# Optimization experiments

Hardware: AMD Instinct MI355X
Metric: run time of the kernel (lower is better)

The kernel has to match this reference:

```python
import jax, jax.numpy as jnp
import numpy as np

HEADS = 20
HEAD_DIM = 64
IP_WEIGHT = 1.0

def _sdpa(q, k, v):
    # q: [b,h,sq,d], k/v: [b,h,skv,d]
    scale = 1.0 / np.sqrt(q.shape[-1])
    logits = jnp.einsum('bhqd,bhkd->bhqk', q, k) * scale
    probs = jax.nn.softmax(logits, axis=-1)
    return jnp.einsum('bhqk,bhkd->bhqd', probs, v)

def _split_heads(t, b, h, d):
    return t.reshape(b, -1, h, d).transpose(0, 2, 1, 3)

def setup_inputs() -> dict:
    key = jax.random.key(0)
    ks = jax.random.split(key, 10)
    B, S, D, C, T = 4, 4096, 1280, 2048, 16
    def w(k, fan_in, shape):
        return jax.random.normal(k, shape, dtype=jnp.float32) / np.sqrt(fan_in)
    return {
        'x': jax.random.normal(ks[0], (B, S, D), dtype=jnp.float32),
        'context': jax.random.normal(ks[1], (B, 77, C), dtype=jnp.float32),
        'image_emb': jax.random.normal(ks[2], (B, T, C), dtype=jnp.float32),
        'Wq': w(ks[3], D, (D, D)),
        'Wk': w(ks[4], C, (C, D)),
        'Wv': w(ks[5], C, (C, D)),
        'Wk_ip': w(ks[6], C, (C, D)),
        'Wv_ip': w(ks[7], C, (C, D)),
        'Wo': w(ks[8], D, (D, D)),
        'bo': jnp.zeros((D,), dtype=jnp.float32),
    }

def reference(x, context, image_emb, Wq, Wk, Wv, Wk_ip, Wv_ip, Wo, bo):
    b, s, inner = x.shape
    h, d = HEADS, HEAD_DIM
    q = _split_heads(x @ Wq, b, h, d)            # [b,h,s,d]
    k = _split_heads(context @ Wk, b, h, d)      # [b,h,77,d]
    v = _split_heads(context @ Wv, b, h, d)
    out = _sdpa(q, k, v)                         # main cross-attn
    ip_k = _split_heads(image_emb @ Wk_ip, b, h, d)  # [b,h,16,d]
    ip_v = _split_heads(image_emb @ Wv_ip, b, h, d)
    ip_out = _sdpa(q, ip_k, ip_v)                # image-conditioned attn, same q
    out = out + IP_WEIGHT * ip_out
    out = out.transpose(0, 2, 1, 3).reshape(b, s, h * d)
    return out @ Wo + bo
```

## Files before the change

### kernel.cpp

```cpp
#include <hip/hip_runtime.h>
#include <cstdint>

typedef __bf16 bf16;
typedef __bf16 bf16x8 __attribute__((ext_vector_type(8)));
typedef float f32x4 __attribute__((ext_vector_type(4)));

#define MFMA16(a, b, c) __builtin_amdgcn_mfma_f32_16x16x32_bf16((a), (b), (c), 0, 0, 0)
#define GLDS16(g, l)                                                         \
  __builtin_amdgcn_global_load_lds(                                          \
      (__attribute__((address_space(1))) void*)(g),                          \
      (__attribute__((address_space(3))) void*)(l), 16, 0, 0)

__global__ void prep_all(const float* __restrict__ Wq, const float* __restrict__ Wo,
                         const float* __restrict__ Wk, const float* __restrict__ Wv,
                         const float* __restrict__ Wkip, const float* __restrict__ Wvip,
                         bf16* __restrict__ WqT, bf16* __restrict__ WoT,
                         bf16* __restrict__ WkT, bf16* __restrict__ WvT,
                         bf16* __restrict__ WkipT, bf16* __restrict__ WvipT,
                         const float* __restrict__ x, bf16* __restrict__ xb,
                         const float* __restrict__ ctx, bf16* __restrict__ ctxb,
                         const float* __restrict__ img, bf16* __restrict__ imgb) {
  const int z = blockIdx.z;
  const int tx = threadIdx.x, ty = threadIdx.y;
  if (z < 6) {
    const float* src = (z == 0) ? Wq : (z == 1) ? Wo : (z == 2) ? Wk
                      : (z == 3) ? Wv : (z == 4) ? Wkip : Wvip;
    bf16* dst = (z == 0) ? WqT : (z == 1) ? WoT : (z == 2) ? WkT
               : (z == 3) ? WvT : (z == 4) ? WkipT : WvipT;
    const int K = (z < 2) ? 1280 : 2048;
    const int N = 1280;
    __shared__ float t[32][33];
    const int bx = blockIdx.x * 32, by = blockIdx.y * 32;
    if (by >= K) return;
#pragma unroll
    for (int i = 0; i < 32; i += 8)
      t[ty + i][tx] = src[(long)(by + ty + i) * N + bx + tx];
    __syncthreads();
#pragma unroll
    for (int i = 0; i < 32; i += 8)
      dst[(long)(bx + ty + i) * K + by + tx] = (bf16)t[tx][ty + i];
    return;
  }
  const int tid = ty * 32 + tx;
  const int bid = blockIdx.y * 40 + blockIdx.x;
  const float* s;
  bf16* d;
  long base;
  if (z < 10) {
    base = (((long)(z - 6) * 2560 + bid) * 256 + tid) * 8;
    s = x; d = xb;
  } else if (bid < 308) {
    base = ((long)bid * 256 + tid) * 8;
    s = ctx; d = ctxb;
  } else if (bid < 372) {
    base = ((long)(bid - 308) * 256 + tid) * 8;
    s = img; d = imgb;
  } else {
    return;
  }
  float4 a = *(const float4*)(s + base);
  float4 b = *(const float4*)(s + base + 4);
  bf16x8 o;
  o[0] = (bf16)a.x; o[1] = (bf16)a.y; o[2] = (bf16)a.z; o[3] = (bf16)a.w;
  o[4] = (bf16)b.x; o[5] = (bf16)b.y; o[6] = (bf16)b.z; o[7] = (bf16)b.w;
  *(bf16x8*)(d + base) = o;
}

template <bool OUT_BF16, bool HAS_BIAS>
__device__ __forceinline__ void gemm_bt_core(const bf16* A, const bf16* Bt,
                                             void* Cp, const float* bias,
                                             int K, int N, int tm, int tn) {
  __shared__ bf16 Al[3][128 * 32];
  __shared__ bf16 Bl[3][128 * 32];
  const int tid = threadIdx.x;
  const int wave = tid >> 6, lane = tid & 63;
  const int g = lane >> 4, l16 = lane & 15;

  const int sr = lane >> 2;
  const int sc = ((lane & 3) ^ ((lane >> 3) & 3)) * 8;
  const bf16* ga0 = A + (long)(tm + wave * 16 + sr) * K + sc;
  const bf16* ga1 = ga0 + (long)64 * K;
  const bf16* gb0 = Bt + (long)(tn + wave * 16 + sr) * K + sc;
  const bf16* gb1 = gb0 + (long)64 * K;

  f32x4 acc[4][4] = {};
  const int wr = (wave >> 1) * 64, wc = (wave & 1) * 64;
  const int rsw = (g ^ ((l16 >> 1) & 3)) * 8;
  const int paOfs = (wr + l16) * 32 + rsw;
  const int pbOfs = (wc + l16) * 32 + rsw;

  const int NT = K >> 5;

#define STAGE_TILE(t_, b_)                              \
  {                                                     \
    const int kt_ = (t_) << 5;                          \
    GLDS16(ga0 + kt_, &Al[b_][wave * 512]);             \
    GLDS16(ga1 + kt_, &Al[b_][(wave + 4) * 512]);       \
    GLDS16(gb0 + kt_, &Bl[b_][wave * 512]);             \
    GLDS16(gb1 + kt_, &Bl[b_][(wave + 4) * 512]);       \
  }

#define READS(sl_, af_, bf_)                                      \
  {                                                               \
    const bf16* pa_ = &Al[sl_][paOfs];                            \
    const bf16* pb_ = &Bl[sl_][pbOfs];                            \
    _Pragma("unroll") for (int i_ = 0; i_ < 4; i_++)              \
        af_[i_] = *(const bf16x8*)(pa_ + i_ * 16 * 32);           \
    _Pragma("unroll") for (int j_ = 0; j_ < 4; j_++)              \
        bf_[j_] = *(const bf16x8*)(pb_ + j_ * 16 * 32);           \
  }

  STAGE_TILE(0, 0);
  STAGE_TILE(1, 1);
  asm volatile("s_waitcnt vmcnt(4)" ::: "memory");
  asm volatile("s_barrier" ::: "memory");
  bf16x8 afA[4], bfA[4], afB[4], bfB[4];
  READS(0, afA, bfA);
  int slc = 0;

#define GEMM_ITER(t_, afC, bfC, afN, bfN)                         \
  {                                                               \
    asm volatile("s_waitcnt lgkmcnt(0)" ::: "memory");            \
    __builtin_amdgcn_sched_barrier(0);                            \
    if ((t_) + 2 < NT) {                                          \
      const int snx_ = (slc + 2 >= 3) ? slc - 1 : slc + 2;        \
      STAGE_TILE((t_) + 2, snx_);                                 \
      asm volatile("s_waitcnt vmcnt(4)" ::: "memory");            \
    } else if ((t_) + 1 < NT) {                                   \
      asm volatile("s_waitcnt vmcnt(0)" ::: "memory");            \
    }                                                             \
    asm volatile("s_barrier" ::: "memory");                       \
    const int srd_ = (slc + 1 >= 3) ? 0 : slc + 1;                \
    if ((t_) + 1 < NT) READS(srd_, afN, bfN);                     \
    __builtin_amdgcn_sched_barrier(0);                            \
    __builtin_amdgcn_s_setprio(1);                                \
    _Pragma("unroll") for (int i_ = 0; i_ < 4; i_++)              \
        _Pragma("unroll") for (int j_ = 0; j_ < 4; j_++)          \
            acc[i_][j_] = MFMA16(afC[i_], bfC[j_], acc[i_][j_]);  \
    __builtin_amdgcn_s_setprio(0);                                \
    slc = srd_;                                                   \
  }

  for (int t = 0; t < NT; t += 2) {
    GEMM_ITER(t, afA, bfA, afB, bfB);
    GEMM_ITER(t + 1, afB, bfB, afA, bfA);
  }
#undef GEMM_ITER
#undef READS
#undef STAGE_TILE

#pragma unroll
  for (int i = 0; i < 4; i++) {
#pragma unroll
    for (int j = 0; j < 4; j++) {
      const int col = tn + wc + j * 16 + l16;
      float bv = 0.f;
      if (HAS_BIAS) bv = bias[col];
#pragma unroll
      for (int r = 0; r < 4; r++) {
        const long row = (long)tm + wr + i * 16 + g * 4 + r;
        float v = acc[i][j][r] + bv;
        if (OUT_BF16)
          ((bf16*)Cp)[row * N + col] = (bf16)v;
        else
          ((float*)Cp)[row * N + col] = v;
      }
    }
  }
}

__global__ __launch_bounds__(256) void gemm_qproj_small(
    const bf16* __restrict__ xb, const bf16* __restrict__ WqT,
    bf16* __restrict__ qb, const bf16* __restrict__ ctxb,
    const bf16* __restrict__ imgb, const bf16* __restrict__ WkT,
    const bf16* __restrict__ WvT, const bf16* __restrict__ WkipT,
    const bf16* __restrict__ WvipT, bf16* __restrict__ kb,
    bf16* __restrict__ vb, bf16* __restrict__ ipkb, bf16* __restrict__ ipvb) {
  const int i = blockIdx.x;
  const bf16 *A, *Bt;
  bf16* C;
  int K, tm, tn;
  if (i >= 80) {
    const int q = i - 80;
    const int local = q >> 3;
    A = xb; Bt = WqT; C = qb; K = 1280;
    tm = ((q & 7) * 16 + local / 10) * 128;
    tn = (local % 10) * 128;
  } else {
    int z, bx, by;
    if (i < 60) {
      z = i / 30;
      const int r = i % 30;
      bx = r % 3;
      by = r / 3;
    } else {
      z = 2 + (i - 60) / 10;
      bx = 0;
      by = (i - 60) % 10;
    }
    A = (z < 2) ? ctxb : imgb;
    Bt = (z == 0) ? WkT : (z == 1) ? WvT : (z == 2) ? WkipT : WvipT;
    C = (z == 0) ? kb : (z == 1) ? vb : (z == 2) ? ipkb : ipvb;
    K = 2048;
    tm = bx * 128;
    tn = by * 128;
  }
  gemm_bt_core<true, false>(A, Bt, C, nullptr, K, 1280, tm, tn);
}

__global__ __launch_bounds__(256) void gemm_f32out_bias(
    const bf16* __restrict__ A, const bf16* __restrict__ Bt,
    float* __restrict__ C, const float* __restrict__ bias, int K, int N) {
  const int i = blockIdx.x;
  const int local = i >> 3;
  const int tm = ((i & 7) * 16 + local / 10) * 128;
  const int tn = (local % 10) * 128;
  gemm_bt_core<false, true>(A, Bt, C, bias, K, N, tm, tn);
}

__global__ __launch_bounds__(256) void attention_kernel(
    const bf16* __restrict__ q, const bf16* __restrict__ k,
    const bf16* __restrict__ v, const bf16* __restrict__ ipk,
    const bf16* __restrict__ ipv, bf16* __restrict__ out) {
  __shared__ bf16 Kl[96 * 64];
  __shared__ bf16 Vt[64 * 104];
  __shared__ bf16 Pl[4][16 * 104];

  const int b = blockIdx.z, h = blockIdx.y, qblk = blockIdx.x;
  const int tid = threadIdx.x;

  {
    uint32_t* vz = (uint32_t*)Vt;
    for (int i = tid; i < 64 * 104 / 2; i += 256) vz[i] = 0;
  }
  __syncthreads();

  for (int c = tid; c < 77 * 8; c += 256) {
    const int row = c >> 3, d0 = (c & 7) * 8;
    const long src = (long)(b * 77 + row) * 1280 + h * 64 + d0;
    bf16x8 kk = *(const bf16x8*)&k[src];
    *(bf16x8*)&Kl[row * 64 + (d0 ^ ((row & 7) << 3))] = kk;
    bf16x8 vv = *(const bf16x8*)&v[src];
#pragma unroll
    for (int i2 = 0; i2 < 8; i2++) Vt[(d0 + i2) * 104 + row] = vv[i2];
  }
  if (tid < 16 * 8) {
    const int r = tid >> 3, d0 = (tid & 7) * 8;
    const int row = 80 + r;
    const long src = (long)(b * 16 + r) * 1280 + h * 64 + d0;
    bf16x8 kk = *(const bf16x8*)&ipk[src];
    *(bf16x8*)&Kl[row * 64 + (d0 ^ ((row & 7) << 3))] = kk;
    bf16x8 vv = *(const bf16x8*)&ipv[src];
#pragma unroll
    for (int i2 = 0; i2 < 8; i2++) Vt[(d0 + i2) * 104 + row] = vv[i2];
  }
  __syncthreads();

  const int wave = tid >> 6, lane = tid & 63;
  const int g = lane >> 4, l16 = lane & 15;
  const float sc = 0.125f * 1.44269504f;

  for (int it = 0; it < 2; it++) {
    const long qrow = (long)b * 4096 + qblk * 128 + wave * 32 + it * 16;
    bf16x8 qf[2];
#pragma unroll
    for (int ks = 0; ks < 2; ks++)
      qf[ks] = *(const bf16x8*)&q[(qrow + l16) * 1280 + h * 64 + ks * 32 + g * 8];

    f32x4 lt[6];
#pragma unroll
    for (int t = 0; t < 6; t++) {
      f32x4 a = {0.f, 0.f, 0.f, 0.f};
#pragma unroll
      for (int ks = 0; ks < 2; ks++) {
        const int row = t * 16 + l16;
        const int d = (ks * 32 + g * 8) ^ ((row & 7) << 3);
        bf16x8 kb8 = *(const bf16x8*)&Kl[row * 64 + d];
        a = MFMA16(qf[ks], kb8, a);
      }
      lt[t] = a;
    }

    float p[6][4];
#pragma unroll
    for (int r = 0; r < 4; r++) {
      float lv[5], m = -3e38f;
#pragma unroll
      for (int t = 0; t < 5; t++) {
        const int kv = t * 16 + l16;
        lv[t] = (kv < 77) ? lt[t][r] * sc : -3e38f;
        m = fmaxf(m, lv[t]);
      }
      for (int msk = 1; msk < 16; msk <<= 1) m = fmaxf(m, __shfl_xor(m, msk, 16));
      float s = 0.f;
#pragma unroll
      for (int t = 0; t < 5; t++) {
        const float pp = exp2f(lv[t] - m);
        p[t][r] = pp;
        s += pp;
      }
      for (int msk = 1; msk < 16; msk <<= 1) s += __shfl_xor(s, msk, 16);
      const float inv = 1.f / s;
#pragma unroll
      for (int t = 0; t < 5; t++) p[t][r] *= inv;
      const float l5 = lt[5][r] * sc;
      float m2 = l5;
      for (int msk = 1; msk < 16; msk <<= 1) m2 = fmaxf(m2, __shfl_xor(m2, msk, 16));
      const float p5 = exp2f(l5 - m2);
      float s2 = p5;
      for (int msk = 1; msk < 16; msk <<= 1) s2 += __shfl_xor(s2, msk, 16);
      p[5][r] = p5 / s2;
    }

#pragma unroll
    for (int t = 0; t < 6; t++)
#pragma unroll
      for (int r = 0; r < 4; r++)
        Pl[wave][(g * 4 + r) * 104 + t * 16 + l16] = (bf16)p[t][r];
    __syncthreads();

    bf16x8 paf[3];
#pragma unroll
    for (int ks = 0; ks < 3; ks++)
      paf[ks] = *(const bf16x8*)&Pl[wave][l16 * 104 + ks * 32 + g * 8];
#pragma unroll
    for (int n = 0; n < 4; n++) {
      f32x4 o = {0.f, 0.f, 0.f, 0.f};
#pragma unroll
      for (int ks = 0; ks < 3; ks++) {
        bf16x8 vbf = *(const bf16x8*)&Vt[(n * 16 + l16) * 104 + ks * 32 + g * 8];
        o = MFMA16(paf[ks], vbf, o);
      }
#pragma unroll
      for (int r = 0; r < 4; r++)
        out[(qrow + g * 4 + r) * 1280 + h * 64 + n * 16 + l16] = (bf16)o[r];
    }
    __syncthreads();
  }
}

extern "C" void kernel_launch(void* const* d_in, const int* in_sizes, int n_in,
                              void* d_out, int out_size, void* d_ws,
                              size_t ws_size, hipStream_t stream) {
  const float* x = (const float*)d_in[0];
  const float* ctx = (const float*)d_in[1];
  const float* img = (const float*)d_in[2];
  const float* Wq = (const float*)d_in[3];
  const float* Wk = (const float*)d_in[4];
  const float* Wv = (const float*)d_in[5];
  const float* Wkip = (const float*)d_in[6];
  const float* Wvip = (const float*)d_in[7];
  const float* Wo = (const float*)d_in[8];
  const float* bo = (const float*)d_in[9];
  float* out = (float*)d_out;

  bf16* ws = (bf16*)d_ws;
  size_t o = 0;
  auto alloc = [&](size_t n) { bf16* p = ws + o; o += n; return p; };
  bf16* xattn = alloc(16384L * 1280);
  bf16* qb    = alloc(16384L * 1280);
  bf16* WqT   = alloc(1280L * 1280);
  bf16* WoT   = alloc(1280L * 1280);
  bf16* WkT   = alloc(1280L * 2048);
  bf16* WvT   = alloc(1280L * 2048);
  bf16* WkipT = alloc(1280L * 2048);
  bf16* WvipT = alloc(1280L * 2048);
  bf16* ctxb  = alloc(384L * 2048);
  bf16* imgb  = alloc(128L * 2048);
  bf16* kb    = alloc(384L * 1280);
  bf16* vb    = alloc(384L * 1280);
  bf16* ipkb  = alloc(128L * 1280);
  bf16* ipvb  = alloc(128L * 1280);

  prep_all<<<dim3(40, 64, 11), dim3(32, 8), 0, stream>>>(
      Wq, Wo, Wk, Wv, Wkip, Wvip, WqT, WoT, WkT, WvT, WkipT, WvipT, x, xattn,
      ctx, ctxb, img, imgb);

  gemm_qproj_small<<<1360, 256, 0, stream>>>(xattn, WqT, qb, ctxb, imgb, WkT,
                                             WvT, WkipT, WvipT, kb, vb, ipkb,
                                             ipvb);

  attention_kernel<<<dim3(32, 20, 4), 256, 0, stream>>>(qb, kb, vb, ipkb, ipvb,
                                                        xattn);

  gemm_f32out_bias<<<1280, 256, 0, stream>>>(xattn, WoT, out, bo, 1280, 1280);
}
```

Before: 232.2 us.

## Switch projection GEMMs to 256x256 tiles with 512-thread blocks and BK=64

Replaces the 128x128, 256-thread, triple-buffered GEMM core with a 256x256 tile per 512-thread block. It uses K-steps of 64 and double-buffered LDS, and interleaves the next tile's global-to-LDS loads between four MFMA sub-phases. The larger tile raises arithmetic intensity and operand reuse per LDS load. It also adds row guards so the small K/V projections can use the bigger tile. In exchange, grids shrink to 350 and 320 blocks, leaving a partial second wave on 256 CUs. The 128 KB of LDS per block limits occupancy, and the padded small-M tiles read past the logical end of ctx/img rows.

New measurement: 264.3 us. +13.8%, slower.

```diff
diff --git a/kernel.cpp b/kernel.cpp
--- a/kernel.cpp
+++ b/kernel.cpp
@@ -67,109 +67,160 @@
 }
 
 template <bool OUT_BF16, bool HAS_BIAS>
-__device__ __forceinline__ void gemm_bt_core(const bf16* A, const bf16* Bt,
+__device__ __forceinline__ void gemm256_core(const bf16* A, const bf16* Bt,
                                              void* Cp, const float* bias,
-                                             int K, int N, int tm, int tn) {
-  __shared__ bf16 Al[3][128 * 32];
-  __shared__ bf16 Bl[3][128 * 32];
+                                             int K, int N, int tm, int tn,
+                                             int Mlim) {
+  __shared__ bf16 Al[2][16384];
+  __shared__ bf16 Bl[2][16384];
   const int tid = threadIdx.x;
   const int wave = tid >> 6, lane = tid & 63;
   const int g = lane >> 4, l16 = lane & 15;
-
-  const int sr = lane >> 2;
-  const int sc = ((lane & 3) ^ ((lane >> 3) & 3)) * 8;
-  const bf16* ga0 = A + (long)(tm + wave * 16 + sr) * K + sc;
-  const bf16* ga1 = ga0 + (long)64 * K;
-  const bf16* gb0 = Bt + (long)(tn + wave * 16 + sr) * K + sc;
-  const bf16* gb1 = gb0 + (long)64 * K;
-
-  f32x4 acc[4][4] = {};
-  const int wr = (wave >> 1) * 64, wc = (wave & 1) * 64;
-  const int rsw = (g ^ ((l16 >> 1) & 3)) * 8;
-  const int paOfs = (wr + l16) * 32 + rsw;
-  const int pbOfs = (wc + l16) * 32 + rsw;
-
-  const int NT = K >> 5;
-
-#define STAGE_TILE(t_, b_)                              \
-  {                                                     \
-    const int kt_ = (t_) << 5;                          \
-    GLDS16(ga0 + kt_, &Al[b_][wave * 512]);             \
-    GLDS16(ga1 + kt_, &Al[b_][(wave + 4) * 512]);       \
-    GLDS16(gb0 + kt_, &Bl[b_][wave * 512]);             \
-    GLDS16(gb1 + kt_, &Bl[b_][(wave + 4) * 512]);       \
-  }
-
-#define READS(sl_, af_, bf_)                                      \
+  const int wr = wave >> 2, wc = wave & 3;
+
+  const int srow = wave * 16 + (lane >> 3);
+  const int scol = ((lane & 7) ^ ((lane >> 3) & 7)) * 8;
+  const bf16* gA = A + (long)(tm + srow) * K + scol;
+  const bf16* gB = Bt + (long)(tn + srow) * K + scol;
+  const int ldst = wave * 1024;
+
+#define STAGE_HALF(Lb_, gp_, b_, hh_, t_)                         \
   {                                                               \
-    const bf16* pa_ = &Al[sl_][paOfs];                            \
-    const bf16* pb_ = &Bl[sl_][pbOfs];                            \
-    _Pragma("unroll") for (int i_ = 0; i_ < 4; i_++)              \
-        af_[i_] = *(const bf16x8*)(pa_ + i_ * 16 * 32);           \
-    _Pragma("unroll") for (int j_ = 0; j_ < 4; j_++)              \
-        bf_[j_] = *(const bf16x8*)(pb_ + j_ * 16 * 32);           \
-  }
-
-  STAGE_TILE(0, 0);
-  STAGE_TILE(1, 1);
-  asm volatile("s_waitcnt vmcnt(4)" ::: "memory");
+    const bf16* s_ = (gp_) + (long)(hh_) * 128 * K + (t_) * 64;   \
+    GLDS16(s_, &Lb_[b_][(hh_)*8192 + ldst]);                      \
+    GLDS16(s_ + 8 * K, &Lb_[b_][(hh_)*8192 + ldst + 512]);        \
+  }
+
+  const int cs0 = (g ^ (l16 & 7)) * 8;
+  const int cs1 = ((4 + g) ^ (l16 & 7)) * 8;
+  const int aB0 = (wr * 64 + l16) * 64;
+  const int aB1 = aB0 + 8192;
+  const int bB = (wc * 64 + l16) * 64;
+
+  f32x4 acc[8][4] = {};
+  bf16x8 aF[4][2], bF[4][2];
+
+  const int NT = K >> 6;
+
+  STAGE_HALF(Al, gA, 0, 0, 0);
+  STAGE_HALF(Al, gA, 0, 1, 0);
+  STAGE_HALF(Bl, gB, 0, 0, 0);
+  STAGE_HALF(Bl, gB, 0, 1, 0);
+  STAGE_HALF(Al, gA, 1, 0, 1);
+  STAGE_HALF(Bl, gB, 1, 0, 1);
+  STAGE_HALF(Bl, gB, 1, 1, 1);
+  asm volatile("s_waitcnt vmcnt(6)" ::: "memory");
   asm volatile("s_barrier" ::: "memory");
-  bf16x8 afA[4], bfA[4], afB[4], bfB[4];
-  READS(0, afA, bfA);
-  int slc = 0;
-
-#define GEMM_ITER(t_, afC, bfC, afN, bfN)                         \
-  {                                                               \
-    asm volatile("s_waitcnt lgkmcnt(0)" ::: "memory");            \
-    __builtin_amdgcn_sched_barrier(0);                            \
-    if ((t_) + 2 < NT) {                                          \
-      const int snx_ = (slc + 2 >= 3) ? slc - 1 : slc + 2;        \
-      STAGE_TILE((t_) + 2, snx_);                                 \
-      asm volatile("s_waitcnt vmcnt(4)" ::: "memory");            \
-    } else if ((t_) + 1 < NT) {                                   \
-      asm volatile("s_waitcnt vmcnt(0)" ::: "memory");            \
-    }                                                             \
-    asm volatile("s_barrier" ::: "memory");                       \
-    const int srd_ = (slc + 1 >= 3) ? 0 : slc + 1;                \
-    if ((t_) + 1 < NT) READS(srd_, afN, bfN);                     \
-    __builtin_amdgcn_sched_barrier(0);                            \
-    __builtin_amdgcn_s_setprio(1);                                \
-    _Pragma("unroll") for (int i_ = 0; i_ < 4; i_++)              \
-        _Pragma("unroll") for (int j_ = 0; j_ < 4; j_++)          \
-            acc[i_][j_] = MFMA16(afC[i_], bfC[j_], acc[i_][j_]);  \
-    __builtin_amdgcn_s_setprio(0);                                \
-    slc = srd_;                                                   \
-  }
-
-  for (int t = 0; t < NT; t += 2) {
-    GEMM_ITER(t, afA, bfA, afB, bfB);
-    GEMM_ITER(t + 1, afB, bfB, afA, bfA);
-  }
-#undef GEMM_ITER
-#undef READS
-#undef STAGE_TILE
-
-#pragma unroll
-  for (int i = 0; i < 4; i++) {
-#pragma unroll
-    for (int j = 0; j < 4; j++) {
-      const int col = tn + wc + j * 16 + l16;
+
+  for (int t = 0; t < NT; ++t) {
+    const int b = t & 1;
+#pragma unroll
+    for (int mi = 0; mi < 4; ++mi) {
+      aF[mi][0] = *(const bf16x8*)&Al[b][aB0 + mi * 1024 + cs0];
+      aF[mi][1] = *(const bf16x8*)&Al[b][aB0 + mi * 1024 + cs1];
+    }
+#pragma unroll
+    for (int nj = 0; nj < 2; ++nj) {
+      bF[nj][0] = *(const bf16x8*)&Bl[b][bB + nj * 1024 + cs0];
+      bF[nj][1] = *(const bf16x8*)&Bl[b][bB + nj * 1024 + cs1];
+    }
+    if (t + 1 < NT) STAGE_HALF(Al, gA, b ^ 1, 1, t + 1);
+    asm volatile("s_barrier" ::: "memory");
+    asm volatile("s_waitcnt lgkmcnt(0)" ::: "memory");
+    __builtin_amdgcn_sched_barrier(0);
+    __builtin_amdgcn_s_setprio(1);
+#pragma unroll
+    for (int mi = 0; mi < 4; ++mi)
+#pragma unroll
+      for (int nj = 0; nj < 2; ++nj) {
+        acc[mi][nj] = MFMA16(aF[mi][0], bF[nj][0], acc[mi][nj]);
+        acc[mi][nj] = MFMA16(aF[mi][1], bF[nj][1], acc[mi][nj]);
+      }
+    __builtin_amdgcn_s_setprio(0);
+    asm volatile("s_barrier" ::: "memory");
+#pragma unroll
+    for (int nj = 2; nj < 4; ++nj) {
+      bF[nj][0] = *(const bf16x8*)&Bl[b][bB + nj * 1024 + cs0];
+      bF[nj][1] = *(const bf16x8*)&Bl[b][bB + nj * 1024 + cs1];
+    }
+    if (t + 2 < NT) STAGE_HALF(Al, gA, b, 0, t + 2);
+    asm volatile("s_barrier" ::: "memory");
+    asm volatile("s_waitcnt lgkmcnt(0)" ::: "memory");
+    __builtin_amdgcn_sched_barrier(0);
+    __builtin_amdgcn_s_setprio(1);
+#pragma unroll
+    for (int mi = 0; mi < 4; ++mi)
+#pragma unroll
+      for (int nj = 2; nj < 4; ++nj) {
+        acc[mi][nj] = MFMA16(aF[mi][0], bF[nj][0], acc[mi][nj]);
+        acc[mi][nj] = MFMA16(aF[mi][1], bF[nj][1], acc[mi][nj]);
+      }
+    __builtin_amdgcn_s_setprio(0);
+    asm volatile("s_barrier" ::: "memory");
+#pragma unroll
+    for (int mi = 0; mi < 4; ++mi) {
+      aF[mi][0] = *(const bf16x8*)&Al[b][aB1 + mi * 1024 + cs0];
+      aF[mi][1] = *(const bf16x8*)&Al[b][aB1 + mi * 1024 + cs1];
+    }
+    if (t + 2 < NT) STAGE_HALF(Bl, gB, b, 0, t + 2);
+    asm volatile("s_barrier" ::: "memory");
+    asm volatile("s_waitcnt lgkmcnt(0)" ::: "memory");
+    __builtin_amdgcn_sched_barrier(0);
+    __builtin_amdgcn_s_setprio(1);
+#pragma unroll
+    for (int mi = 0; mi < 4; ++mi)
+#pragma unroll
+      for (int nj = 2; nj < 4; ++nj) {
+        acc[4 + mi][nj] = MFMA16(aF[mi][0], bF[nj][0], acc[4 + mi][nj]);
+        acc[4 + mi][nj] = MFMA16(aF[mi][1], bF[nj][1], acc[4 + mi][nj]);
+      }
+    __builtin_amdgcn_s_setprio(0);
+    asm volatile("s_barrier" ::: "memory");
+    if (t + 2 < NT) STAGE_HALF(Bl, gB, b, 1, t + 2);
+    asm volatile("s_barrier" ::: "memory");
+    __builtin_amdgcn_sched_barrier(0);
+    __builtin_amdgcn_s_setprio(1);
+#pragma unroll
+    for (int mi = 0; mi < 4; ++mi)
+#pragma unroll
+      for (int nj = 0; nj < 2; ++nj) {
+        acc[4 + mi][nj] = MFMA16(aF[mi][0], bF[nj][0], acc[4 + mi][nj]);
+        acc[4 + mi][nj] = MFMA16(aF[mi][1], bF[nj][1], acc[4 + mi][nj]);
+      }
+    __builtin_amdgcn_s_setprio(0);
+    if (t + 2 < NT) {
+      asm volatile("s_waitcnt vmcnt(6)" ::: "memory");
+    } else if (t + 1 < NT) {
+      asm volatile("s_waitcnt vmcnt(0)" ::: "memory");
+    }
+    asm volatile("s_barrier" ::: "memory");
+  }
+#undef STAGE_HALF
+
+#pragma unroll
+  for (int mi = 0; mi < 8; ++mi) {
+    const int rb = (mi < 4) ? (wr * 64 + mi * 16) : (128 + wr * 64 + (mi - 4) * 16);
+#pragma unroll
+    for (int nj = 0; nj < 4; ++nj) {
+      const int col = tn + wc * 64 + nj * 16 + l16;
       float bv = 0.f;
       if (HAS_BIAS) bv = bias[col];
 #pragma unroll
-      for (int r = 0; r < 4; r++) {
-        const long row = (long)tm + wr + i * 16 + g * 4 + r;
-        float v = acc[i][j][r] + bv;
-        if (OUT_BF16)
-          ((bf16*)Cp)[row * N + col] = (bf16)v;
-        else
-          ((float*)Cp)[row * N + col] = v;
-      }
-    }
-  }
-}
-
-__global__ __launch_bounds__(256) void gemm_qproj_small(
+      for (int r = 0; r < 4; ++r) {
+        const long row = (long)tm + rb + g * 4 + r;
+        if (row < Mlim) {
+          float v = acc[mi][nj][r] + bv;
+          if (OUT_BF16)
+            ((bf16*)Cp)[row * N + col] = (bf16)v;
+          else
+            ((float*)Cp)[row * N + col] = v;
+        }
+      }
+    }
+  }
+}
+
+__global__ __launch_bounds__(512, 2) void gemm_qproj_small(
     const bf16* __restrict__ xb, const bf16* __restrict__ WqT,
     bf16* __restrict__ qb, const bf16* __restrict__ ctxb,
     const bf16* __restrict__ imgb, const bf16* __restrict__ WkT,
@@ -179,43 +230,42 @@
   const int i = blockIdx.x;
   const bf16 *A, *Bt;
   bf16* C;
-  int K, tm, tn;
-  if (i >= 80) {
-    const int q = i - 80;
+  int K, tm, tn, Mlim;
+  if (i >= 30) {
+    const int q = i - 30;
     const int local = q >> 3;
-    A = xb; Bt = WqT; C = qb; K = 1280;
-    tm = ((q & 7) * 16 + local / 10) * 128;
-    tn = (local % 10) * 128;
+    A = xb; Bt = WqT; C = qb; K = 1280; Mlim = 1 << 30;
+    tm = ((q & 7) * 8 + local / 5) * 256;
+    tn = (local % 5) * 256;
   } else {
     int z, bx, by;
-    if (i < 60) {
-      z = i / 30;
-      const int r = i % 30;
-      bx = r % 3;
-      by = r / 3;
+    if (i < 20) {
+      z = i / 10;
+      const int r = i % 10;
+      bx = r / 5; by = r % 5;
     } else {
-      z = 2 + (i - 60) / 10;
-      bx = 0;
-      by = (i - 60) % 10;
+      z = 2 + (i - 20) / 5;
+      bx = 0; by = (i - 20) % 5;
     }
     A = (z < 2) ? ctxb : imgb;
     Bt = (z == 0) ? WkT : (z == 1) ? WvT : (z == 2) ? WkipT : WvipT;
     C = (z == 0) ? kb : (z == 1) ? vb : (z == 2) ? ipkb : ipvb;
     K = 2048;
-    tm = bx * 128;
-    tn = by * 128;
-  }
-  gemm_bt_core<true, false>(A, Bt, C, nullptr, K, 1280, tm, tn);
-}
-
-__global__ __launch_bounds__(256) void gemm_f32out_bias(
+    tm = bx * 256;
+    tn = by * 256;
+    Mlim = (z < 2) ? 384 : 128;
+  }
+  gemm256_core<true, false>(A, Bt, C, nullptr, K, 1280, tm, tn, Mlim);
+}
+
+__global__ __launch_bounds__(512, 2) void gemm_f32out_bias(
     const bf16* __restrict__ A, const bf16* __restrict__ Bt,
     float* __restrict__ C, const float* __restrict__ bias, int K, int N) {
   const int i = blockIdx.x;
   const int local = i >> 3;
-  const int tm = ((i & 7) * 16 + local / 10) * 128;
-  const int tn = (local % 10) * 128;
-  gemm_bt_core<false, true>(A, Bt, C, bias, K, N, tm, tn);
+  const int tm = ((i & 7) * 8 + local / 5) * 256;
+  const int tn = (local % 5) * 256;
+  gemm256_core<false, true>(A, Bt, C, bias, K, N, tm, tn, 1 << 30);
 }
 
 __global__ __launch_bounds__(256) void attention_kernel(
@@ -376,12 +426,12 @@
       Wq, Wo, Wk, Wv, Wkip, Wvip, WqT, WoT, WkT, WvT, WkipT, WvipT, x, xattn,
       ctx, ctxb, img, imgb);
 
-  gemm_qproj_small<<<1360, 256, 0, stream>>>(xattn, WqT, qb, ctxb, imgb, WkT,
-                                             WvT, WkipT, WvipT, kb, vb, ipkb,
-                                             ipvb);
+  gemm_qproj_small<<<350, 512, 0, stream>>>(xattn, WqT, qb, ctxb, imgb, WkT,
+                                            WvT, WkipT, WvipT, kb, vb, ipkb,
+                                            ipvb);
 
   attention_kernel<<<dim3(32, 20, 4), 256, 0, stream>>>(qb, kb, vb, ipkb, ipvb,
                                                         xattn);
 
-  gemm_f32out_bias<<<1280, 256, 0, stream>>>(xattn, WoT, out, bo, 1280, 1280);
-}
+  gemm_f32out_bias<<<320, 512, 0, stream>>>(xattn, WoT, out, bo, 1280, 1280);
+}
```

## Fuse fp32-to-bf16 conversion of x into the Q-projection GEMM A-tile load

Applied to the files above, without the earlier changes.

Drops the separate pass that converts x from fp32 to bf16 in the prep kernel. The Q-projection GEMM now loads fp32 x tiles straight into registers, converts them, and writes them to LDS inside a new triple-buffered pipeline, while B still goes global-to-LDS directly. This removes a full write and re-read of a bf16 copy of x. In exchange the GEMM reads twice the A bytes per tile, uses more registers, and has a more complex wait-count schedule; launch bounds are set to 3 blocks per SM.

After: 344.4 us. 48.3% more time.

```diff
diff --git a/kernel.cpp b/kernel.cpp
--- a/kernel.cpp
+++ b/kernel.cpp
@@ -17,7 +17,6 @@
                          bf16* __restrict__ WqT, bf16* __restrict__ WoT,
                          bf16* __restrict__ WkT, bf16* __restrict__ WvT,
                          bf16* __restrict__ WkipT, bf16* __restrict__ WvipT,
-                         const float* __restrict__ x, bf16* __restrict__ xb,
                          const float* __restrict__ ctx, bf16* __restrict__ ctxb,
                          const float* __restrict__ img, bf16* __restrict__ imgb) {
   const int z = blockIdx.z;
@@ -46,10 +45,7 @@
   const float* s;
   bf16* d;
   long base;
-  if (z < 10) {
-    base = (((long)(z - 6) * 2560 + bid) * 256 + tid) * 8;
-    s = x; d = xb;
-  } else if (bid < 308) {
+  if (bid < 308) {
     base = ((long)bid * 256 + tid) * 8;
     s = ctx; d = ctxb;
   } else if (bid < 372) {
@@ -169,43 +165,164 @@
   }
 }
 
-__global__ __launch_bounds__(256) void gemm_qproj_small(
-    const bf16* __restrict__ xb, const bf16* __restrict__ WqT,
+__device__ __forceinline__ void gemm_qproj_core(const float* A, const bf16* Bt,
+                                                bf16* Cp, int K, int N,
+                                                int tm, int tn) {
+  __shared__ bf16 Al[3][128 * 32];
+  __shared__ bf16 Bl[3][128 * 32];
+  const int tid = threadIdx.x;
+  const int wave = tid >> 6, lane = tid & 63;
+  const int g = lane >> 4, l16 = lane & 15;
+
+  const int sr = lane >> 2;
+  const int sc = ((lane & 3) ^ ((lane >> 3) & 3)) * 8;
+  const float* gaf0 = A + (long)(tm + wave * 16 + sr) * K + sc;
+  const float* gaf1 = gaf0 + (long)64 * K;
+  const bf16* gb0 = Bt + (long)(tn + wave * 16 + sr) * K + sc;
+  const bf16* gb1 = gb0 + (long)64 * K;
+
+  f32x4 acc[4][4] = {};
+  const int wr = (wave >> 1) * 64, wc = (wave & 1) * 64;
+  const int rsw = (g ^ ((l16 >> 1) & 3)) * 8;
+  const int paOfs = (wr + l16) * 32 + rsw;
+  const int pbOfs = (wc + l16) * 32 + rsw;
+
+  const int NT = K >> 5;
+
+#define LOADA(t_, R_)                              \
+  {                                                \
+    const int kt_ = (t_) << 5;                     \
+    R_[0] = *(const float4*)(gaf0 + kt_);          \
+    R_[1] = *(const float4*)(gaf0 + kt_ + 4);      \
+    R_[2] = *(const float4*)(gaf1 + kt_);          \
+    R_[3] = *(const float4*)(gaf1 + kt_ + 4);      \
+  }
+#define WRITEA(b_, R_)                                                   \
+  {                                                                      \
+    bf16x8 w0_, w1_;                                                     \
+    w0_[0] = (bf16)R_[0].x; w0_[1] = (bf16)R_[0].y;                      \
+    w0_[2] = (bf16)R_[0].z; w0_[3] = (bf16)R_[0].w;                      \
+    w0_[4] = (bf16)R_[1].x; w0_[5] = (bf16)R_[1].y;                      \
+    w0_[6] = (bf16)R_[1].z; w0_[7] = (bf16)R_[1].w;                      \
+    w1_[0] = (bf16)R_[2].x; w1_[1] = (bf16)R_[2].y;                      \
+    w1_[2] = (bf16)R_[2].z; w1_[3] = (bf16)R_[2].w;                      \
+    w1_[4] = (bf16)R_[3].x; w1_[5] = (bf16)R_[3].y;                      \
+    w1_[6] = (bf16)R_[3].z; w1_[7] = (bf16)R_[3].w;                      \
+    *(bf16x8*)&Al[b_][wave * 512 + lane * 8] = w0_;                      \
+    *(bf16x8*)&Al[b_][(wave + 4) * 512 + lane * 8] = w1_;                \
+  }
+#define STAGEB(t_, b_)                                  \
+  {                                                     \
+    const int kt_ = (t_) << 5;                          \
+    GLDS16(gb0 + kt_, &Bl[b_][wave * 512]);             \
+    GLDS16(gb1 + kt_, &Bl[b_][(wave + 4) * 512]);       \
+  }
+#define READS(sl_, af_, bf_)                                      \
+  {                                                               \
+    const bf16* pa_ = &Al[sl_][paOfs];                            \
+    const bf16* pb_ = &Bl[sl_][pbOfs];                            \
+    _Pragma("unroll") for (int i_ = 0; i_ < 4; i_++)              \
+        af_[i_] = *(const bf16x8*)(pa_ + i_ * 16 * 32);           \
+    _Pragma("unroll") for (int j_ = 0; j_ < 4; j_++)              \
+        bf_[j_] = *(const bf16x8*)(pb_ + j_ * 16 * 32);           \
+  }
+
+  float4 ra[4], rb[4];
+  LOADA(0, ra);
+  STAGEB(0, 0);
+  asm volatile("s_waitcnt vmcnt(0)" ::: "memory");
+  WRITEA(0, ra);
+  LOADA(1, rb);
+  STAGEB(1, 1);
+  asm volatile("s_waitcnt lgkmcnt(0)" ::: "memory");
+  asm volatile("s_barrier" ::: "memory");
+  bf16x8 afA[4], bfA[4], afB[4], bfB[4];
+  READS(0, afA, bfA);
+  int slc = 0;
+
+#define GEMM_ITER_Q(t_, afC, bfC, afN, bfN, raC, raN)                    \
+  {                                                                      \
+    asm volatile("s_waitcnt lgkmcnt(0)" ::: "memory");                   \
+    __builtin_amdgcn_sched_barrier(0);                                   \
+    const int srd_ = (slc + 1 >= 3) ? 0 : slc + 1;                       \
+    if ((t_) + 2 < NT) {                                                 \
+      const int snx_ = (slc + 2 >= 3) ? slc - 1 : slc + 2;               \
+      LOADA((t_) + 2, raN);                                              \
+      STAGEB((t_) + 2, snx_);                                            \
+      asm volatile("s_waitcnt vmcnt(6)" ::: "memory");                   \
+    } else if ((t_) + 1 < NT) {                                          \
+      asm volatile("s_waitcnt vmcnt(0)" ::: "memory");                   \
+    }                                                                    \
+    if ((t_) + 1 < NT) {                                                 \
+      WRITEA(srd_, raC);                                                 \
+      asm volatile("s_waitcnt lgkmcnt(0)" ::: "memory");                 \
+    }                                                                    \
+    asm volatile("s_barrier" ::: "memory");                              \
+    if ((t_) + 1 < NT) READS(srd_, afN, bfN);                            \
+    __builtin_amdgcn_sched_barrier(0);                                   \
+    __builtin_amdgcn_s_setprio(1);                                       \
+    _Pragma("unroll") for (int i_ = 0; i_ < 4; i_++)                     \
+        _Pragma("unroll") for (int j_ = 0; j_ < 4; j_++)                 \
+            acc[i_][j_] = MFMA16(afC[i_], bfC[j_], acc[i_][j_]);         \
+    __builtin_amdgcn_s_setprio(0);                                       \
+    slc = srd_;                                                          \
+  }
+
+  for (int t = 0; t < NT; t += 2) {
+    GEMM_ITER_Q(t, afA, bfA, afB, bfB, rb, ra);
+    GEMM_ITER_Q(t + 1, afB, bfB, afA, bfA, ra, rb);
+  }
+#undef GEMM_ITER_Q
+#undef READS
+#undef STAGEB
+#undef WRITEA
+#undef LOADA
+
+#pragma unroll
+  for (int i = 0; i < 4; i++) {
+#pragma unroll
+    for (int j = 0; j < 4; j++) {
+      const int col = tn + wc + j * 16 + l16;
+#pragma unroll
+      for (int r = 0; r < 4; r++) {
+        const long row = (long)tm + wr + i * 16 + g * 4 + r;
+        Cp[row * N + col] = (bf16)acc[i][j][r];
+      }
+    }
+  }
+}
+
+__global__ __launch_bounds__(256, 3) void gemm_qproj_small(
+    const float* __restrict__ x, const bf16* __restrict__ WqT,
     bf16* __restrict__ qb, const bf16* __restrict__ ctxb,
     const bf16* __restrict__ imgb, const bf16* __restrict__ WkT,
     const bf16* __restrict__ WvT, const bf16* __restrict__ WkipT,
     const bf16* __restrict__ WvipT, bf16* __restrict__ kb,
     bf16* __restrict__ vb, bf16* __restrict__ ipkb, bf16* __restrict__ ipvb) {
   const int i = blockIdx.x;
-  const bf16 *A, *Bt;
-  bf16* C;
-  int K, tm, tn;
   if (i >= 80) {
     const int q = i - 80;
     const int local = q >> 3;
-    A = xb; Bt = WqT; C = qb; K = 1280;
-    tm = ((q & 7) * 16 + local / 10) * 128;
-    tn = (local % 10) * 128;
+    const int tm = ((q & 7) * 16 + local / 10) * 128;
+    const int tn = (local % 10) * 128;
+    gemm_qproj_core(x, WqT, qb, 1280, 1280, tm, tn);
+    return;
+  }
+  int z, bx, by;
+  if (i < 60) {
+    z = i / 30;
+    const int r = i % 30;
+    bx = r % 3;
+    by = r / 3;
   } else {
-    int z, bx, by;
-    if (i < 60) {
-      z = i / 30;
-      const int r = i % 30;
-      bx = r % 3;
-      by = r / 3;
-    } else {
-      z = 2 + (i - 60) / 10;
-      bx = 0;
-      by = (i - 60) % 10;
-    }
-    A = (z < 2) ? ctxb : imgb;
-    Bt = (z == 0) ? WkT : (z == 1) ? WvT : (z == 2) ? WkipT : WvipT;
-    C = (z == 0) ? kb : (z == 1) ? vb : (z == 2) ? ipkb : ipvb;
-    K = 2048;
-    tm = bx * 128;
-    tn = by * 128;
-  }
-  gemm_bt_core<true, false>(A, Bt, C, nullptr, K, 1280, tm, tn);
+    z = 2 + (i - 60) / 10;
+    bx = 0;
+    by = (i - 60) % 10;
+  }
+  const bf16* A = (z < 2) ? ctxb : imgb;
+  const bf16* Bt = (z == 0) ? WkT : (z == 1) ? WvT : (z == 2) ? WkipT : WvipT;
+  bf16* C = (z == 0) ? kb : (z == 1) ? vb : (z == 2) ? ipkb : ipvb;
+  gemm_bt_core<true, false>(A, Bt, C, nullptr, 2048, 1280, bx * 128, by * 128);
 }
 
 __global__ __launch_bounds__(256) void gemm_f32out_bias(
@@ -372,11 +489,11 @@
   bf16* ipkb  = alloc(128L * 1280);
   bf16* ipvb  = alloc(128L * 1280);
 
-  prep_all<<<dim3(40, 64, 11), dim3(32, 8), 0, stream>>>(
-      Wq, Wo, Wk, Wv, Wkip, Wvip, WqT, WoT, WkT, WvT, WkipT, WvipT, x, xattn,
+  prep_all<<<dim3(40, 64, 7), dim3(32, 8), 0, stream>>>(
+      Wq, Wo, Wk, Wv, Wkip, Wvip, WqT, WoT, WkT, WvT, WkipT, WvipT,
       ctx, ctxb, img, imgb);
 
-  gemm_qproj_small<<<1360, 256, 0, stream>>>(xattn, WqT, qb, ctxb, imgb, WkT,
+  gemm_qproj_small<<<1360, 256, 0, stream>>>(x, WqT, qb, ctxb, imgb, WkT,
                                              WvT, WkipT, WvipT, kb, vb, ipkb,
                                              ipvb);
 
```
